# Optimization experiments

Measured on AMD Instinct MI355X. Metric: run time of the kernel, lower is better.

Reference implementation:

```python
import jax, jax.numpy as jnp
import numpy as np

NEG_SLOPE = 0.01  # torch F.leaky_relu default


def setup_inputs() -> dict:
    key = jax.random.key(0)
    ks = jax.random.split(key, 6)
    N, d, E, L = 100000, 64, 1600000, 3
    edge_index = jax.random.randint(ks[0], (2, E), 0, N, dtype=jnp.int64 if jax.config.jax_enable_x64 else jnp.int32)
    edge_weight = jax.random.uniform(ks[1], (E,), jnp.float32)
    emb = jax.random.normal(ks[2], (N, d), jnp.float32) * 0.1
    scale = 1.0 / np.sqrt(d)  # xavier-ish
    W1 = jax.random.normal(ks[3], (L, d, d), jnp.float32) * scale
    b1 = jnp.zeros((L, d), jnp.float32)
    W2 = jax.random.normal(ks[4], (L, d, d), jnp.float32) * scale
    b2 = jnp.zeros((L, d), jnp.float32)
    return dict(edge_index=edge_index, edge_weight=edge_weight, emb=emb,
                W1=W1, b1=b1, W2=W2, b2=b2)


def reference(edge_index, edge_weight, emb, W1, b1, W2, b2):
    # RecSysGNN.forward (eval mode: dropout is identity)
    N = emb.shape[0]
    frm, to = edge_index[0], edge_index[1]
    # symmetric-normalization coefficients (same edge_index every layer -> hoist)
    deg = jnp.zeros((N,), emb.dtype).at[to].add(jnp.ones_like(edge_weight, emb.dtype))
    dis = jnp.where(deg > 0, 1.0 / jnp.sqrt(jnp.maximum(deg, 1.0)), 0.0)
    norm = dis[frm] * dis[to] * edge_weight  # [E]

    emb0 = emb
    x = emb0
    L = W1.shape[0]
    for l in range(L):  # fixed small layer count
        xj = x[frm]          # [E, d] gather source
        xi = x[to]           # [E, d] gather target
        # message: norm * (lin_1(x_j) + lin_2(x_j * x_i))
        msg = norm[:, None] * ((xj @ W1[l].T + b1[l]) + ((xj * xi) @ W2[l].T + b2[l]))
        agg = jnp.zeros_like(x).at[to].add(msg)  # scatter-add aggregation
        x = jax.nn.leaky_relu(agg + (x @ W1[l].T + b1[l]), NEG_SLOPE)
    out = jnp.concatenate([emb0, x], axis=-1)  # note: original only appends emb0 and final emb
    return (emb0, out)
```

## Files before the change

kernel.cpp:

```cpp
#include <hip/hip_runtime.h>
#include <hip/hip_fp16.h>
#include <math.h>

#define D 64
#define NPB 64
#define MAXFB 1568
#define CHUNK 4096
#define CHUNK_H 16384
#define SCAP 2048
#define GTP 68
#define FMASK 0x1FFFFu
#define FLAGB 0x800000u

typedef __attribute__((ext_vector_type(8))) _Float16 f16x8;
typedef __attribute__((ext_vector_type(4))) float f32x4;

static inline size_t align256(size_t x) { return (x + 255) & ~(size_t)255; }

__global__ __launch_bounds__(1024) void k_hist(const int* __restrict__ to, int E, int NFB,
                                               unsigned* __restrict__ bcnt) {
    __shared__ unsigned h[MAXFB];
    int t = threadIdx.x;
    for (int i = t; i < MAXFB; i += 1024) h[i] = 0;
    __syncthreads();
    int base = blockIdx.x * CHUNK_H;
    int cnt = E - base; if (cnt > CHUNK_H) cnt = CHUNK_H;
    for (int j = t; j < cnt; j += 1024)
        atomicAdd(&h[((unsigned)to[base + j]) >> 6], 1u);
    __syncthreads();
    for (int i = t; i < NFB; i += 1024) {
        unsigned c = h[i];
        if (c) atomicAdd(&bcnt[i], c);
    }
}

__global__ __launch_bounds__(1024) void k_scanb(const unsigned* __restrict__ bcnt, int NFB,
                                                int* __restrict__ fine_base, int* __restrict__ gcur) {
    __shared__ unsigned sh[1024];
    int t = threadIdx.x;
    int i0 = 2 * t, i1 = 2 * t + 1;
    unsigned a0 = (i0 < NFB) ? bcnt[i0] : 0u;
    unsigned a1 = (i1 < NFB) ? bcnt[i1] : 0u;
    unsigned sum = a0 + a1;
    sh[t] = sum;
    __syncthreads();
    for (int ofs = 1; ofs < 1024; ofs <<= 1) {
        unsigned v = (t >= ofs) ? sh[t - ofs] : 0u;
        __syncthreads();
        sh[t] += v;
        __syncthreads();
    }
    unsigned eb = sh[t] - sum;
    if (i0 < NFB) { fine_base[i0] = (int)eb; gcur[i0] = (int)eb; }
    if (i1 < NFB) { fine_base[i1] = (int)(eb + a0); gcur[i1] = (int)(eb + a0); }
    if (t == 0) fine_base[NFB] = (int)sh[1023];
}

__global__ __launch_bounds__(1024) void k_cfill(
        const int* __restrict__ frm, const int* __restrict__ to, const float* __restrict__ w,
        int E, int NFB, int* __restrict__ gcur, int2* __restrict__ ert) {
    __shared__ int2 stage[CHUNK];
    __shared__ unsigned short sfb[CHUNK];
    __shared__ unsigned hist[MAXFB];
    __shared__ unsigned scanE[MAXFB];
    __shared__ unsigned lbase[MAXFB];
    __shared__ unsigned sh[1024];
    int t = threadIdx.x;
    int base = blockIdx.x * CHUNK;
    int cnt = E - base; if (cnt > CHUNK) cnt = CHUNK;
    for (int b = t; b < MAXFB; b += 1024) hist[b] = 0;
    __syncthreads();
    int2 rec[4]; int fbv[4];
#pragma unroll
    for (int i = 0; i < 4; ++i) {
        int e = base + t + i * 1024;
        fbv[i] = -1;
        if (e < E) {
            int f = frm[e], tt = to[e];
            rec[i].x = f | ((tt & (NPB - 1)) << 20);
            rec[i].y = __float_as_int(w[e]);
            int fb = tt >> 6;
            fbv[i] = fb;
            atomicAdd(&hist[fb], 1u);
        }
    }
    __syncthreads();
    int i0 = 2 * t, i1 = 2 * t + 1;
    unsigned a0 = (i0 < MAXFB) ? hist[i0] : 0u;
    unsigned a1 = (i1 < MAXFB) ? hist[i1] : 0u;
    unsigned sum = a0 + a1;
    sh[t] = sum;
    __syncthreads();
    for (int ofs = 1; ofs < 1024; ofs <<= 1) {
        unsigned v = (t >= ofs) ? sh[t - ofs] : 0u;
        __syncthreads();
        sh[t] += v;
        __syncthreads();
    }
    unsigned eb = sh[t] - sum;
    if (i0 < MAXFB) scanE[i0] = eb;
    if (i1 < MAXFB) scanE[i1] = eb + a0;
    __syncthreads();
    for (int b = t; b < NFB; b += 1024) {
        unsigned c = hist[b];
        if (c) lbase[b] = (unsigned)atomicAdd(&gcur[b], (int)c);
        hist[b] = 0;
    }
    __syncthreads();
#pragma unroll
    for (int i = 0; i < 4; ++i) {
        if (fbv[i] >= 0) {
            unsigned loc = atomicAdd(&hist[fbv[i]], 1u);
            unsigned slot = scanE[fbv[i]] + loc;
            stage[slot] = rec[i];
            sfb[slot] = (unsigned short)fbv[i];
        }
    }
    __syncthreads();
    for (int j = t; j < cnt; j += 1024) {
        int fb = sfb[j];
        ert[(int)lbase[fb] + (j - (int)scanE[fb])] = stage[j];
    }
}

__global__ __launch_bounds__(256) void k_bsort(
        const int2* __restrict__ ert, const int* __restrict__ fine_base,
        int N, int NFB, int2* __restrict__ er, int* __restrict__ rowptr,
        float* __restrict__ dis) {
    __shared__ int2 st[SCAP];
    __shared__ int2 st2[SCAP];
    __shared__ unsigned cnt[NPB];
    __shared__ unsigned dcount[NPB];
    __shared__ unsigned cbase[NPB];
    __shared__ float dl[NPB];
    int fb = blockIdx.x;
    int b0 = fine_base[fb], b1 = fine_base[fb + 1];
    int len = b1 - b0;
    int t = threadIdx.x;
    if (t < NPB) cnt[t] = 0;
    __syncthreads();
    if (len <= SCAP) {
        for (int j = t; j < len; j += 256) {
            int2 r = ert[b0 + j];
            st[j] = r;
            atomicAdd(&cnt[(r.x >> 20) & 63], 1u);
        }
        __syncthreads();
        if (t < NPB) {
            unsigned c = cnt[t];
            dcount[t] = c;
            dl[t] = c ? 1.0f / sqrtf((float)c) : 0.0f;
        }
        __syncthreads();
        if (t == 0) {
            unsigned run = 0;
            for (int i = 0; i < NPB; ++i) { cbase[i] = run; run += cnt[i]; cnt[i] = 0; }
        }
        __syncthreads();
        for (int j = t; j < len; j += 256) {
            int2 r = st[j];
            int n = (r.x >> 20) & 63;
            unsigned loc = atomicAdd(&cnt[n], 1u);
            int2 o;
            o.x = (int)((r.x & FMASK) | ((unsigned)n << 17) |
                        ((loc == dcount[n] - 1) ? FLAGB : 0u));
            o.y = __float_as_int(__int_as_float(r.y) * dl[n]);
            st2[cbase[n] + loc] = o;
        }
        __syncthreads();
        for (int j = t; j < len; j += 256) er[b0 + j] = st2[j];
    } else {
        for (int j = t; j < len; j += 256)
            atomicAdd(&cnt[(ert[b0 + j].x >> 20) & 63], 1u);
        __syncthreads();
        if (t < NPB) {
            unsigned c = cnt[t];
            dcount[t] = c;
            dl[t] = c ? 1.0f / sqrtf((float)c) : 0.0f;
        }
        __syncthreads();
        if (t == 0) {
            unsigned run = 0;
            for (int i = 0; i < NPB; ++i) { cbase[i] = run; run += cnt[i]; cnt[i] = 0; }
        }
        __syncthreads();
        for (int j = t; j < len; j += 256) {
            int2 r = ert[b0 + j];
            int n = (r.x >> 20) & 63;
            unsigned loc = atomicAdd(&cnt[n], 1u);
            int2 o;
            o.x = (int)((r.x & FMASK) | ((unsigned)n << 17) |
                        ((loc == dcount[n] - 1) ? FLAGB : 0u));
            o.y = __float_as_int(__int_as_float(r.y) * dl[n]);
            er[b0 + (int)cbase[n] + (int)loc] = o;
        }
        __syncthreads();
    }
    int nbase = fb * NPB;
    if (t < NPB && nbase + t < N) {
        rowptr[nbase + t] = b0 + (int)cbase[t];
        dis[nbase + t] = dl[t];
    }
    if (fb == NFB - 1 && t == 0) rowptr[N] = b1;
}

__global__ void k_wprep(const float* __restrict__ W1, const float* __restrict__ W2,
                        int Lnum, f16x8* __restrict__ wf) {
    int idx = blockIdx.x * blockDim.x + threadIdx.x;
    if (idx >= Lnum * 16 * 64) return;
    int lane = idx & 63;
    int fr = (idx >> 6) & 15;
    int l = idx >> 10;
    int mat = fr >> 3, nt = (fr >> 1) & 3, ks = fr & 1;
    int j = nt * 16 + (lane & 15);
    int kb = ((lane >> 4) << 3) + ks * 32;
    const float* src = (mat ? W2 : W1) + (size_t)l * D * D + j * D + kb;
    f16x8 v;
#pragma unroll
    for (int q = 0; q < 8; ++q) v[q] = (_Float16)src[q];
    wf[idx] = v;
}

__global__ void k_prep(int2* __restrict__ er, const float* __restrict__ dis, int E,
                       const float* __restrict__ emb, __half* __restrict__ x,
                       float* __restrict__ out, int N) {
    int total = E + N * 16;
    int st = gridDim.x * blockDim.x;
    const float4* e4 = (const float4*)emb;
    float4* o4 = (float4*)out;
    __half2* xh = (__half2*)x;
    for (int i = blockIdx.x * blockDim.x + threadIdx.x; i < total; i += st) {
        if (i < E) {
            int2 r = er[i];
            er[i].y = __float_as_int(__int_as_float(r.y) * dis[(unsigned)r.x & FMASK]);
        } else {
            int j = i - E;
            float4 v = e4[j];
            o4[j] = v;
            int n = j >> 4, c = j & 15;
            o4[(size_t)N * 16 + (size_t)n * 32 + c] = v;
            xh[2 * j]     = __floats2half2_rn(v.x, v.y);
            xh[2 * j + 1] = __floats2half2_rn(v.z, v.w);
        }
    }
}

__global__ void k_sums(const int2* __restrict__ er, const int* __restrict__ rowptr,
                       int N, float* __restrict__ s) {
    int n = blockIdx.x * blockDim.x + threadIdx.x;
    if (n >= N) return;
    int e0 = rowptr[n], e1 = rowptr[n + 1];
    float sv = 0.0f;
    for (int e = e0; e < e1; ++e) sv += __int_as_float(er[e].y);
    s[n] = sv;
}

__device__ __forceinline__ void flushf(float* __restrict__ gtw, int tl, int c32, bool hib,
                                       float& g0, float& g1) {
    float s0 = g0 + __shfl_xor(g0, 32);
    float s1 = g1 + __shfl_xor(g1, 32);
    if (!hib) {
        float2* p = (float2*)&gtw[tl * GTP + (c32 << 1)];
        float2 v; v.x = s0; v.y = s1;
        *p = v;
    }
    g0 = 0.0f; g1 = 0.0f;
}

__global__ __launch_bounds__(256, 6) void k_flayer(
        const int* __restrict__ rowptr, const int2* __restrict__ er,
        const __half* __restrict__ xin, const f16x8* __restrict__ wfg,
        const float* __restrict__ s,
        const float* __restrict__ b1, const float* __restrict__ b2,
        int N, float* __restrict__ outf, __half* __restrict__ outh, int ostride) {
    __shared__ __align__(16) float gt[4][16][GTP];
    int tid = threadIdx.x;
    int lane = tid & 63, wv = tid >> 6;
    int tb = (blockIdx.x * 4 + wv) * 16;
    if (tb >= N) return;
    float* gtw = &gt[wv][0][0];
#pragma unroll
    for (int p = 0; p < 16; ++p) gtw[p * GTP + lane] = 0.0f;
    int e = rowptr[tb], eend = rowptr[tb + 16];
    const char* xbase = (const char*)xin;
    int c32 = lane & 31;
    bool hib = lane >= 32;
    unsigned coff = (unsigned)c32 << 2;
    if (e < eend) {
        float g0 = 0.0f, g1 = 0.0f;
        if (e & 1) {
            int2 r = er[e];
            unsigned rx = (unsigned)r.x;
            float nv = hib ? 0.0f : __int_as_float(r.y);
            __half2 hv = *(const __half2*)(xbase + ((size_t)(rx & FMASK) << 7) + coff);
            g0 = fmaf(nv, __low2float(hv), g0);
            g1 = fmaf(nv, __high2float(hv), g1);
            if (rx & FLAGB) flushf(gtw, (rx >> 17) & 15, c32, hib, g0, g1);
            ++e;
        }
        while (e + 16 <= eend) {
            int4 rc[8];
#pragma unroll
            for (int k = 0; k < 8; ++k) rc[k] = *(const int4*)&er[e + 2 * k];
            __half2 hv[8];
            float nv[8];
#pragma unroll
            for (int k = 0; k < 8; ++k) {
                unsigned rx = (unsigned)(hib ? rc[k].z : rc[k].x);
                nv[k] = __int_as_float(hib ? rc[k].w : rc[k].y);
                hv[k] = *(const __half2*)(xbase + ((size_t)(rx & FMASK) << 7) + coff);
            }
#pragma unroll
            for (int k = 0; k < 8; ++k) {
                unsigned rxl = (unsigned)rc[k].x, rxh = (unsigned)rc[k].z;
                float c0 = nv[k] * __low2float(hv[k]);
                float c1 = nv[k] * __high2float(hv[k]);
                if (!((rxl | rxh) & FLAGB)) {
                    g0 += c0; g1 += c1;
                } else if (rxl & FLAGB) {
                    if (!hib) { g0 += c0; g1 += c1; }
                    flushf(gtw, (rxl >> 17) & 15, c32, hib, g0, g1);
                    if (hib) { g0 += c0; g1 += c1; }
                    if (rxh & FLAGB) flushf(gtw, (rxh >> 17) & 15, c32, hib, g0, g1);
                } else {
                    g0 += c0; g1 += c1;
                    flushf(gtw, (rxh >> 17) & 15, c32, hib, g0, g1);
                }
            }
            e += 16;
        }
        while (e + 2 <= eend) {
            int4 rc = *(const int4*)&er[e];
            unsigned rxl = (unsigned)rc.x, rxh = (unsigned)rc.z;
            unsigned rx = hib ? rxh : rxl;
            float nv = __int_as_float(hib ? rc.w : rc.y);
            __half2 hvv = *(const __half2*)(xbase + ((size_t)(rx & FMASK) << 7) + coff);
            float c0 = nv * __low2float(hvv);
            float c1 = nv * __high2float(hvv);
            if (!((rxl | rxh) & FLAGB)) {
                g0 += c0; g1 += c1;
            } else if (rxl & FLAGB) {
                if (!hib) { g0 += c0; g1 += c1; }
                flushf(gtw, (rxl >> 17) & 15, c32, hib, g0, g1);
                if (hib) { g0 += c0; g1 += c1; }
                if (rxh & FLAGB) flushf(gtw, (rxh >> 17) & 15, c32, hib, g0, g1);
            } else {
                g0 += c0; g1 += c1;
                flushf(gtw, (rxh >> 17) & 15, c32, hib, g0, g1);
            }
            e += 2;
        }
        if (e < eend) {
            int2 r = er[e];
            unsigned rx = (unsigned)r.x;
            float nv = hib ? 0.0f : __int_as_float(r.y);
            __half2 hvv = *(const __half2*)(xbase + ((size_t)(rx & FMASK) << 7) + coff);
            g0 = fmaf(nv, __low2float(hvv), g0);
            g1 = fmaf(nv, __high2float(hvv), g1);
            if (rx & FLAGB) flushf(gtw, (rx >> 17) & 15, c32, hib, g0, g1);
        }
    }
    int L = lane & 15, H = lane >> 4;
    f16x8 a1[2], a2[2];
#pragma unroll
    for (int ks = 0; ks < 2; ++ks) {
        const float* gp = &gt[wv][L][(H << 3) + ks * 32];
        f32x4 g0v = *(const f32x4*)gp;
        f32x4 g1v = *(const f32x4*)(gp + 4);
        f16x8 xv = *(const f16x8*)(xin + (((size_t)(tb + L)) << 6) + (H << 3) + ks * 32);
        f16x8 h1v, h2v;
#pragma unroll
        for (int q = 0; q < 4; ++q) {
            float gq = g0v[q], xq = (float)xv[q];
            h1v[q] = (_Float16)(gq + xq);
            h2v[q] = (_Float16)(gq * xq);
        }
#pragma unroll
        for (int q = 0; q < 4; ++q) {
            float gq = g1v[q], xq = (float)xv[4 + q];
            h1v[4 + q] = (_Float16)(gq + xq);
            h2v[4 + q] = (_Float16)(gq * xq);
        }
        a1[ks] = h1v; a2[ks] = h2v;
    }
    float sr[4];
#pragma unroll
    for (int r = 0; r < 4; ++r) sr[r] = s[tb + (H << 2) + r];
#pragma unroll
    for (int nt = 0; nt < 4; ++nt) {
        f16x8 w0 = wfg[(nt * 2 + 0) * 64 + lane];
        f16x8 w1 = wfg[(nt * 2 + 1) * 64 + lane];
        f16x8 w2 = wfg[(8 + nt * 2 + 0) * 64 + lane];
        f16x8 w3 = wfg[(8 + nt * 2 + 1) * 64 + lane];
        float bb1 = b1[nt * 16 + L], bb2 = b2[nt * 16 + L];
        f32x4 acc;
#pragma unroll
        for (int r = 0; r < 4; ++r) acc[r] = (sr[r] + 1.0f) * bb1 + sr[r] * bb2;
        acc = __builtin_amdgcn_mfma_f32_16x16x32_f16(a1[0], w0, acc, 0, 0, 0);
        acc = __builtin_amdgcn_mfma_f32_16x16x32_f16(a1[1], w1, acc, 0, 0, 0);
        acc = __builtin_amdgcn_mfma_f32_16x16x32_f16(a2[0], w2, acc, 0, 0, 0);
        acc = __builtin_amdgcn_mfma_f32_16x16x32_f16(a2[1], w3, acc, 0, 0, 0);
#pragma unroll
        for (int r = 0; r < 4; ++r) {
            float v = acc[r];
            v = v > 0.0f ? v : 0.01f * v;
            int row = tb + (H << 2) + r;
            if (outf) outf[(size_t)row * ostride + nt * 16 + L] = v;
            else      outh[((size_t)row << 6) + nt * 16 + L] = __float2half(v);
        }
        __builtin_amdgcn_sched_barrier(0);
    }
}

extern "C" void kernel_launch(void* const* d_in, const int* in_sizes, int n_in,
                              void* d_out, int out_size, void* d_ws, size_t ws_size,
                              hipStream_t stream) {
    const int* eidx = (const int*)d_in[0];
    const float* w = (const float*)d_in[1];
    const float* emb = (const float*)d_in[2];
    const float* W1 = (const float*)d_in[3];
    const float* b1 = (const float*)d_in[4];
    const float* W2 = (const float*)d_in[5];
    const float* b2 = (const float*)d_in[6];

    int E = in_sizes[1];
    int N = in_sizes[2] / D;
    int L = in_sizes[3] / (D * D);
    const int* frm = eidx;
    const int* to = eidx + E;
    int NFB = (N + NPB - 1) / NPB;

    char* ws = (char*)d_ws;
    size_t off = 0;
    __half* x0 = (__half*)(ws + off);      off += align256((size_t)N * D * 2);
    __half* x1 = (__half*)(ws + off);      off += align256((size_t)N * D * 2);
    int2* er = (int2*)(ws + off);          off += align256((size_t)E * 8);
    int2* ert = (int2*)(ws + off);         off += align256((size_t)E * 8);
    int* rowptr = (int*)(ws + off);        off += align256((size_t)(N + 1) * 4);
    float* dis = (float*)(ws + off);       off += align256((size_t)N * 4);
    float* s = (float*)(ws + off);         off += align256((size_t)N * 4);
    unsigned* bcnt = (unsigned*)(ws + off);off += align256((size_t)MAXFB * 4);
    int* fine_base = (int*)(ws + off);     off += align256((size_t)(MAXFB + 1) * 4);
    int* gcur = (int*)(ws + off);          off += align256((size_t)MAXFB * 4);
    f16x8* wf = (f16x8*)(ws + off);        off += align256((size_t)L * 16 * 64 * 16);

    float* out = (float*)d_out;

    hipMemsetAsync(bcnt, 0, (size_t)MAXFB * 4, stream);
    k_wprep<<<(L * 16 * 64 + 255) / 256, 256, 0, stream>>>(W1, W2, L, wf);
    k_hist<<<(E + CHUNK_H - 1) / CHUNK_H, 1024, 0, stream>>>(to, E, NFB, bcnt);
    k_scanb<<<1, 1024, 0, stream>>>(bcnt, NFB, fine_base, gcur);
    k_cfill<<<(E + CHUNK - 1) / CHUNK, 1024, 0, stream>>>(frm, to, w, E, NFB, gcur, ert);
    k_bsort<<<NFB, 256, 0, stream>>>(ert, fine_base, N, NFB, er, rowptr, dis);
    k_prep<<<2048, 256, 0, stream>>>(er, dis, E, emb, x0, out, N);
    k_sums<<<(N + 255) / 256, 256, 0, stream>>>(er, rowptr, N, s);

    __half* xin = x0;
    __half* xalt = x1;
    int nblk = (N + 63) / 64;
    for (int l = 0; l < L; ++l) {
        float* outf = nullptr;
        __half* outh = xalt;
        int ostride = D;
        if (l == L - 1) {
            outf = out + (size_t)N * D + D;
            outh = nullptr;
            ostride = 2 * D;
        }
        k_flayer<<<nblk, 256, 0, stream>>>(rowptr, er, xin,
                                           wf + (size_t)l * 16 * 64, s,
                                           b1 + (size_t)l * D, b2 + (size_t)l * D,
                                           N, outf, outh, ostride);
        __half* t = xin; xin = xalt; xalt = t;
    }
}
```

Measured before the change: 236.2 us.

## Pre-shift source byte offsets in edge records and launch one wave per tile

The packed edge record now stores the source node index pre-shifted into a byte offset (index<<7) with the flag in bit 0 and the local target in bits 1-4. The gather then forms its address with a single mask instead of mask, shift and 64-bit extend. The layer kernel also moves from 4-wave blocks sharing a 4-tile LDS buffer to 64-thread blocks that each handle one 16-node tile, which lets the scheduler place waves more freely. The risk is more block-launch overhead, and 32-bit offsets cap the node count at about 33M.

```diff
diff --git a/kernel.cpp b/kernel.cpp
--- a/kernel.cpp
+++ b/kernel.cpp
@@ -10,7 +10,6 @@
 #define SCAP 2048
 #define GTP 68
 #define FMASK 0x1FFFFu
-#define FLAGB 0x800000u
 
 typedef __attribute__((ext_vector_type(8))) _Float16 f16x8;
 typedef __attribute__((ext_vector_type(4))) float f32x4;
@@ -162,8 +161,8 @@
             int n = (r.x >> 20) & 63;
             unsigned loc = atomicAdd(&cnt[n], 1u);
             int2 o;
-            o.x = (int)((r.x & FMASK) | ((unsigned)n << 17) |
-                        ((loc == dcount[n] - 1) ? FLAGB : 0u));
+            o.x = (int)((((unsigned)r.x & FMASK) << 7) | (((unsigned)n & 15u) << 1) |
+                        ((loc == dcount[n] - 1) ? 1u : 0u));
             o.y = __float_as_int(__int_as_float(r.y) * dl[n]);
             st2[cbase[n] + loc] = o;
         }
@@ -189,8 +188,8 @@
             int n = (r.x >> 20) & 63;
             unsigned loc = atomicAdd(&cnt[n], 1u);
             int2 o;
-            o.x = (int)((r.x & FMASK) | ((unsigned)n << 17) |
-                        ((loc == dcount[n] - 1) ? FLAGB : 0u));
+            o.x = (int)((((unsigned)r.x & FMASK) << 7) | (((unsigned)n & 15u) << 1) |
+                        ((loc == dcount[n] - 1) ? 1u : 0u));
             o.y = __float_as_int(__int_as_float(r.y) * dl[n]);
             er[b0 + (int)cbase[n] + (int)loc] = o;
         }
@@ -232,7 +231,7 @@
     for (int i = blockIdx.x * blockDim.x + threadIdx.x; i < total; i += st) {
         if (i < E) {
             int2 r = er[i];
-            er[i].y = __float_as_int(__int_as_float(r.y) * dis[(unsigned)r.x & FMASK]);
+            er[i].y = __float_as_int(__int_as_float(r.y) * dis[(unsigned)r.x >> 7]);
         } else {
             int j = i - E;
             float4 v = e4[j];
@@ -267,18 +266,16 @@
     g0 = 0.0f; g1 = 0.0f;
 }
 
-__global__ __launch_bounds__(256, 6) void k_flayer(
+__global__ __launch_bounds__(64, 8) void k_flayer(
         const int* __restrict__ rowptr, const int2* __restrict__ er,
         const __half* __restrict__ xin, const f16x8* __restrict__ wfg,
         const float* __restrict__ s,
         const float* __restrict__ b1, const float* __restrict__ b2,
         int N, float* __restrict__ outf, __half* __restrict__ outh, int ostride) {
-    __shared__ __align__(16) float gt[4][16][GTP];
-    int tid = threadIdx.x;
-    int lane = tid & 63, wv = tid >> 6;
-    int tb = (blockIdx.x * 4 + wv) * 16;
-    if (tb >= N) return;
-    float* gtw = &gt[wv][0][0];
+    __shared__ __align__(16) float gt[16 * GTP];
+    int lane = threadIdx.x;
+    int tb = blockIdx.x * 16;
+    float* gtw = gt;
 #pragma unroll
     for (int p = 0; p < 16; ++p) gtw[p * GTP + lane] = 0.0f;
     int e = rowptr[tb], eend = rowptr[tb + 16];
@@ -292,10 +289,10 @@
             int2 r = er[e];
             unsigned rx = (unsigned)r.x;
             float nv = hib ? 0.0f : __int_as_float(r.y);
-            __half2 hv = *(const __half2*)(xbase + ((size_t)(rx & FMASK) << 7) + coff);
+            __half2 hv = *(const __half2*)(xbase + (rx & ~0x7Fu) + coff);
             g0 = fmaf(nv, __low2float(hv), g0);
             g1 = fmaf(nv, __high2float(hv), g1);
-            if (rx & FLAGB) flushf(gtw, (rx >> 17) & 15, c32, hib, g0, g1);
+            if (rx & 1u) flushf(gtw, (rx >> 1) & 15, c32, hib, g0, g1);
             ++e;
         }
         while (e + 16 <= eend) {
@@ -308,23 +305,23 @@
             for (int k = 0; k < 8; ++k) {
                 unsigned rx = (unsigned)(hib ? rc[k].z : rc[k].x);
                 nv[k] = __int_as_float(hib ? rc[k].w : rc[k].y);
-                hv[k] = *(const __half2*)(xbase + ((size_t)(rx & FMASK) << 7) + coff);
+                hv[k] = *(const __half2*)(xbase + (rx & ~0x7Fu) + coff);
             }
 #pragma unroll
             for (int k = 0; k < 8; ++k) {
                 unsigned rxl = (unsigned)rc[k].x, rxh = (unsigned)rc[k].z;
                 float c0 = nv[k] * __low2float(hv[k]);
                 float c1 = nv[k] * __high2float(hv[k]);
-                if (!((rxl | rxh) & FLAGB)) {
+                if (!((rxl | rxh) & 1u)) {
                     g0 += c0; g1 += c1;
-                } else if (rxl & FLAGB) {
+                } else if (rxl & 1u) {
                     if (!hib) { g0 += c0; g1 += c1; }
-                    flushf(gtw, (rxl >> 17) & 15, c32, hib, g0, g1);
+                    flushf(gtw, (rxl >> 1) & 15, c32, hib, g0, g1);
                     if (hib) { g0 += c0; g1 += c1; }
-                    if (rxh & FLAGB) flushf(gtw, (rxh >> 17) & 15, c32, hib, g0, g1);
+                    if (rxh & 1u) flushf(gtw, (rxh >> 1) & 15, c32, hib, g0, g1);
                 } else {
                     g0 += c0; g1 += c1;
-                    flushf(gtw, (rxh >> 17) & 15, c32, hib, g0, g1);
+                    flushf(gtw, (rxh >> 1) & 15, c32, hib, g0, g1);
                 }
             }
             e += 16;
@@ -334,19 +331,19 @@
             unsigned rxl = (unsigned)rc.x, rxh = (unsigned)rc.z;
             unsigned rx = hib ? rxh : rxl;
             float nv = __int_as_float(hib ? rc.w : rc.y);
-            __half2 hvv = *(const __half2*)(xbase + ((size_t)(rx & FMASK) << 7) + coff);
+            __half2 hvv = *(const __half2*)(xbase + (rx & ~0x7Fu) + coff);
             float c0 = nv * __low2float(hvv);
             float c1 = nv * __high2float(hvv);
-            if (!((rxl | rxh) & FLAGB)) {
+            if (!((rxl | rxh) & 1u)) {
                 g0 += c0; g1 += c1;
-            } else if (rxl & FLAGB) {
+            } else if (rxl & 1u) {
                 if (!hib) { g0 += c0; g1 += c1; }
-                flushf(gtw, (rxl >> 17) & 15, c32, hib, g0, g1);
+                flushf(gtw, (rxl >> 1) & 15, c32, hib, g0, g1);
                 if (hib) { g0 += c0; g1 += c1; }
-                if (rxh & FLAGB) flushf(gtw, (rxh >> 17) & 15, c32, hib, g0, g1);
+                if (rxh & 1u) flushf(gtw, (rxh >> 1) & 15, c32, hib, g0, g1);
             } else {
                 g0 += c0; g1 += c1;
-                flushf(gtw, (rxh >> 17) & 15, c32, hib, g0, g1);
+                flushf(gtw, (rxh >> 1) & 15, c32, hib, g0, g1);
             }
             e += 2;
         }
@@ -354,17 +351,17 @@
             int2 r = er[e];
             unsigned rx = (unsigned)r.x;
             float nv = hib ? 0.0f : __int_as_float(r.y);
-            __half2 hvv = *(const __half2*)(xbase + ((size_t)(rx & FMASK) << 7) + coff);
+            __half2 hvv = *(const __half2*)(xbase + (rx & ~0x7Fu) + coff);
             g0 = fmaf(nv, __low2float(hvv), g0);
             g1 = fmaf(nv, __high2float(hvv), g1);
-            if (rx & FLAGB) flushf(gtw, (rx >> 17) & 15, c32, hib, g0, g1);
+            if (rx & 1u) flushf(gtw, (rx >> 1) & 15, c32, hib, g0, g1);
         }
     }
     int L = lane & 15, H = lane >> 4;
     f16x8 a1[2], a2[2];
 #pragma unroll
     for (int ks = 0; ks < 2; ++ks) {
-        const float* gp = &gt[wv][L][(H << 3) + ks * 32];
+        const float* gp = &gtw[L * GTP + (H << 3) + ks * 32];
         f32x4 g0v = *(const f32x4*)gp;
         f32x4 g1v = *(const f32x4*)(gp + 4);
         f16x8 xv = *(const f16x8*)(xin + (((size_t)(tb + L)) << 6) + (H << 3) + ks * 32);
@@ -457,7 +454,7 @@
 
     __half* xin = x0;
     __half* xalt = x1;
-    int nblk = (N + 63) / 64;
+    int ntiles = (N + 15) / 16;
     for (int l = 0; l < L; ++l) {
         float* outf = nullptr;
         __half* outh = xalt;
@@ -467,10 +464,10 @@
             outh = nullptr;
             ostride = 2 * D;
         }
-        k_flayer<<<nblk, 256, 0, stream>>>(rowptr, er, xin,
-                                           wf + (size_t)l * 16 * 64, s,
-                                           b1 + (size_t)l * D, b2 + (size_t)l * D,
-                                           N, outf, outh, ostride);
+        k_flayer<<<ntiles, 64, 0, stream>>>(rowptr, er, xin,
+                                            wf + (size_t)l * 16 * 64, s,
+                                            b1 + (size_t)l * D, b2 + (size_t)l * D,
+                                            N, outf, outh, ostride);
         __half* t = xin; xin = xalt; xalt = t;
     }
 }
```

New measurement: 207.5 us. 12.1% less time.
